# Kernel tuning notes

Measured on AMD Instinct MI355X. Metric: run time of the kernel, lower is better.

The kernel has to match this reference:

```python
import jax, jax.numpy as jnp
import numpy as np

B, N, FEAT, H, E, L = 4096, 64, 32, 128, 4, 3  # batch, node_num, node feat, hidden_dim, edge_dim, hidden_num


def setup_inputs() -> dict:
    key = jax.random.key(0)
    ks = jax.random.split(key, 12)
    s = 0.05
    x = jax.random.normal(ks[0], (B, N, FEAT), dtype=jnp.float32)
    adj = jax.random.uniform(ks[1], (B, E, N, N), dtype=jnp.float32)
    # per-node input/output embeddings (stacked over node index)
    in_w = jax.random.normal(ks[2], (N, FEAT, H), dtype=jnp.float32) * s
    in_b = jax.random.normal(ks[3], (N, H), dtype=jnp.float32) * s
    out_w = jax.random.normal(ks[4], (N, H, FEAT), dtype=jnp.float32) * s
    out_b = jax.random.normal(ks[5], (N, FEAT), dtype=jnp.float32) * s
    # relational GC weights per layer: (L, E, H, H) and bias (L, E, 1, H)
    gc_w = jax.random.normal(ks[6], (L, E, H, H), dtype=jnp.float32) * s
    gc_b = jax.random.normal(ks[7], (L, E, 1, H), dtype=jnp.float32) * s
    # GRU params, gate order [r, z, n] like torch
    w_ih = jax.random.normal(ks[8], (3 * H, H), dtype=jnp.float32) * s
    w_hh = jax.random.normal(ks[9], (3 * H, H), dtype=jnp.float32) * s
    b_ih = jax.random.normal(ks[10], (3 * H,), dtype=jnp.float32) * s
    b_hh = jax.random.normal(ks[11], (3 * H,), dtype=jnp.float32) * s
    return {"x": x, "adj": adj, "in_w": in_w, "in_b": in_b, "out_w": out_w,
            "out_b": out_b, "gc_w": gc_w, "gc_b": gc_b, "w_ih": w_ih,
            "w_hh": w_hh, "b_ih": b_ih, "b_hh": b_hh}


def _gru_step(xf, h, w_ih, w_hh, b_ih, b_hh):
    # xf, h: (B*N, H); single-timestep torch GRU cell
    gi = xf @ w_ih.T + b_ih
    gh = h @ w_hh.T + b_hh
    i_r, i_z, i_n = jnp.split(gi, 3, axis=-1)
    h_r, h_z, h_n = jnp.split(gh, 3, axis=-1)
    r = jax.nn.sigmoid(i_r + h_r)
    z = jax.nn.sigmoid(i_z + h_z)
    n = jnp.tanh(i_n + r * h_n)
    return (1.0 - z) * n + z * h


def reference(x, adj, in_w, in_b, out_w, out_b, gc_w, gc_b, w_ih, w_hh, b_ih, b_hh):
    # per-node input embedding: (B, N, FEAT) -> (B, N, H)
    h = jnp.einsum('bnd,ndh->bnh', x, in_w) + in_b
    hidden = h.reshape(-1, H)  # initial GRU hidden = embedded input
    cur = h
    for i in range(L):
        # relational GCN: per-edge-type projection + adjacency matmul + bias + relu + mean over edge types
        support = jnp.einsum('bid,edh->beih', cur, gc_w[i])
        out = jnp.einsum('beij,bejh->beih', adj, support) + gc_b[i]
        out = jax.nn.relu(out)
        agg = jnp.mean(out, axis=1)  # (B, N, H)
        hidden = _gru_step(agg.reshape(-1, H), hidden, w_ih, w_hh, b_ih, b_hh)
        cur = hidden.reshape(B, N, H)
    # per-node output embedding, zero-padded back to hidden width
    feats = jnp.einsum('bnh,nhd->bnd', cur, out_w) + out_b  # (B, N, FEAT)
    return jnp.pad(feats, ((0, 0), (0, 0), (0, H - FEAT)))
```

## Files before the change

kernel.cpp:

```cpp
#include <hip/hip_runtime.h>
#include <cstdint>

#define NBATCH 4096
#define NNODE  64
#define FEAT   32
#define H      128
#define NE     4
#define NL     3

typedef __attribute__((ext_vector_type(8))) short short8;
typedef __attribute__((ext_vector_type(4))) short short4v;
typedef __attribute__((ext_vector_type(4))) float f32x4;
typedef __attribute__((ext_vector_type(2))) float f32x2;
typedef unsigned long long u64;
typedef unsigned short ushort;

#define IMG_GC_ELEMS   (128 * 64)
#define IMG_GRU_ELEMS  (48 * 128)
#define IMG_GC_BYTES   (24 * IMG_GC_ELEMS * 2)
#define IMG_GRU_BYTES  (16 * IMG_GRU_ELEMS * 2)
#define WS_W_BYTES     (IMG_GC_BYTES + IMG_GRU_BYTES)
#define WIMG_SHORTS    (WS_W_BYTES / 2)
#define ADJ_IMG_ELEMS  4096
#define WS_FULL ((size_t)WS_W_BYTES + (size_t)NBATCH * NE * ADJ_IMG_ELEMS * 2)

__device__ __forceinline__ ushort f2b(float f) {
  union { float f; unsigned u; } v; v.f = f;
  unsigned u = v.u + 0x7FFFu + ((v.u >> 16) & 1u);
  return (ushort)(u >> 16);
}
__device__ __forceinline__ float b2f(ushort s) {
  union { unsigned u; float f; } v; v.u = ((unsigned)s) << 16;
  return v.f;
}
__device__ __forceinline__ unsigned cvtpk(float lo, float hi) {
  unsigned r;
  asm volatile("v_cvt_pk_bf16_f32 %0, %1, %2" : "=v"(r) : "v"(lo), "v"(hi));
  return r;
}
__device__ __forceinline__ u64 pk4(float a, float b, float c, float d) {
  return (u64)cvtpk(a, b) | ((u64)cvtpk(c, d) << 32);
}
__device__ __forceinline__ float sigm(float v) { return 1.0f / (1.0f + __expf(-v)); }
__device__ __forceinline__ float tanh_(float v) {
  v = fminf(fmaxf(v, -15.f), 15.f);
  float e = __expf(-2.f * v);
  return (1.f - e) / (1.f + e);
}
__device__ __forceinline__ int gidx128(int r, int g) { return r * 128 + ((g ^ (r & 7)) << 3); }
__device__ __forceinline__ int idx128(int r, int k) { return gidx128(r, k >> 3) + (k & 7); }
__device__ __forceinline__ int gidx64(int r, int g) { return r * 64 + (((g ^ (r & 7)) & 7) << 3); }

__device__ __forceinline__ short8 pack8f(const float* v) {
  union { unsigned u[4]; short8 s; } r;
  r.u[0] = cvtpk(v[0], v[1]); r.u[1] = cvtpk(v[2], v[3]);
  r.u[2] = cvtpk(v[4], v[5]); r.u[3] = cvtpk(v[6], v[7]);
  return r.s;
}

__device__ __forceinline__ void gll16(const void* g, void* l) {
  __builtin_amdgcn_global_load_lds(
      (const __attribute__((address_space(1))) unsigned int*)g,
      (__attribute__((address_space(3))) unsigned int*)l, 16, 0, 0);
}

#define STAGE(dst, src, NIT)                                             \
  do {                                                                   \
    _Pragma("unroll")                                                    \
    for (int it_ = 0; it_ < (NIT); ++it_) {                              \
      int off_ = (it_ * 4 + w) * 1024;                                   \
      gll16((const char*)(src) + off_ + lane * 16, (char*)(dst) + off_); \
    }                                                                    \
  } while (0)

#define MFMA16(A, B, C) __builtin_amdgcn_mfma_f32_16x16x32_bf16((A), (B), (C), 0, 0, 0)
#define GFRAG(base, off) (*(const short8*)&(base)[(off)])

__global__ __launch_bounds__(256, 2) void k_prep(
    const float* __restrict__ gc_w, const float* __restrict__ w_ih,
    const float* __restrict__ w_hh, ushort* __restrict__ ws)
{
  const int t = threadIdx.x;
  if (blockIdx.x < 24) {
    const int blk = blockIdx.x;
    const int kh = blk & 1, e = (blk >> 1) & 3, l = blk >> 3;
    const float* We = gc_w + (size_t)(l * NE + e) * H * H;
    ushort* dst = ws + (size_t)blk * IMG_GC_ELEMS;
    #pragma unroll
    for (int it = 0; it < 4; ++it) {
      int idx = t + it * 256;
      int r = idx >> 3, g = idx & 7;
      float v[8];
      #pragma unroll
      for (int j = 0; j < 8; ++j) v[j] = We[(kh * 64 + g * 8 + j) * H + r];
      *(short8*)&dst[gidx64(r, g)] = pack8f(v);
    }
  } else {
    const int blk = blockIdx.x - 24;
    const int c = blk & 7, m = blk >> 3;
    const float* Mat = m ? w_hh : w_ih;
    ushort* dst = ws + WIMG_SHORTS - IMG_GRU_BYTES / 2 + (size_t)blk * IMG_GRU_ELEMS;
    #pragma unroll
    for (int it = 0; it < 3; ++it) {
      int idx = t + it * 256;
      int rr = idx >> 4, g = idx & 15;
      int mrow = (rr >> 4) * H + 16 * c + (rr & 15);
      float v[8];
      #pragma unroll
      for (int j = 0; j < 8; ++j) v[j] = Mat[mrow * H + g * 8 + j];
      *(short8*)&dst[gidx128(rr, g)] = pack8f(v);
    }
  }
}

template <bool ADJIMG>
__global__ __launch_bounds__(256, 2) void k_inemb(
    const float* __restrict__ x, const float* __restrict__ in_w,
    const float* __restrict__ in_b, const float* __restrict__ adj,
    ushort* __restrict__ ws, float* __restrict__ out)
{
  __shared__ float s_wt[FEAT * H];
  __shared__ float s_x[64 * FEAT];
  const int t = threadIdx.x;
  const int n = blockIdx.x >> 6, bt = blockIdx.x & 63, b0 = bt * 64;
  const float* wsrc = in_w + (size_t)n * FEAT * H;
  #pragma unroll
  for (int it = 0; it < 4; ++it) {
    int i4 = t + it * 256;
    *(f32x4*)&s_wt[i4 * 4] = *(const f32x4*)&wsrc[i4 * 4];
  }
  {
    int r = t >> 2, q = t & 3;
    const float* xs = x + ((size_t)(b0 + r) * NNODE + n) * FEAT;
    *(f32x4*)&s_x[r * 32 + q * 8]     = *(const f32x4*)&xs[q * 8];
    *(f32x4*)&s_x[r * 32 + q * 8 + 4] = *(const f32x4*)&xs[q * 8 + 4];
  }
  __syncthreads();
  const int h2 = t & 63, rp = t >> 6;
  const float bi0 = in_b[n * H + 2 * h2], bi1 = in_b[n * H + 2 * h2 + 1];
  #pragma unroll 1
  for (int m = 0; m < 16; ++m) {
    int r = rp + 4 * m;
    float a0 = bi0, a1 = bi1;
    #pragma unroll
    for (int d = 0; d < 32; ++d) {
      float xv = s_x[r * 32 + d];
      f32x2 wv = *(const f32x2*)&s_wt[d * H + 2 * h2];
      a0 += xv * wv.x; a1 += xv * wv.y;
    }
    unsigned p = cvtpk(a0, a1);
    ushort* tail = (ushort*)(out + ((size_t)(b0 + r) * NNODE + n) * H + 64);
    *(unsigned*)(tail + 2 * h2) = p;
  }
  if (ADJIMG) {
    const float* ab = adj + (size_t)blockIdx.x * NE * NNODE * NNODE;
    ushort* dst = ws + WIMG_SHORTS + (size_t)blockIdx.x * NE * ADJ_IMG_ELEMS;
    #pragma unroll 1
    for (int q = 0; q < 8; ++q) {
      int gi = t + q * 256;
      int e = gi >> 9, idx = gi & 511, r = idx >> 3, g = idx & 7;
      const float* src = ab + e * 4096 + r * 64 + g * 8;
      float v[8];
      #pragma unroll
      for (int j = 0; j < 8; ++j) v[j] = src[j];
      *(short8*)&dst[e * ADJ_IMG_ELEMS + gidx64(r, g)] = pack8f(v);
    }
  }
}

template <bool ADJIMG>
__global__ __launch_bounds__(256, 2) void k_main(
    const float* __restrict__ adj,
    const float* __restrict__ gc_b,
    const float* __restrict__ b_ih, const float* __restrict__ b_hh,
    const ushort* __restrict__ wimg,
    float* __restrict__ out)
{
  __shared__ ushort s_u[8192];
  __shared__ ushort s_adj[4096];
  __shared__ float  s_bias[1280];

  const int t = threadIdx.x, b = blockIdx.x;
  const int w = t >> 6, lane = t & 63, lr = lane & 15, lq = lane >> 4;
  const int wm = w & 1, wn = w >> 1;
  float* outb = out + (size_t)b * NNODE * H;
  const ushort* img_gru = wimg + WIMG_SHORTS - IMG_GRU_BYTES / 2;
  const ushort* aimg = wimg + WIMG_SHORTS + (size_t)b * NE * ADJ_IMG_ELEMS;

  short8 cur[2][4];
  #pragma unroll
  for (int mt = 0; mt < 2; ++mt)
    #pragma unroll
    for (int ks = 0; ks < 4; ++ks)
      cur[mt][ks] = *(const short8*)((const ushort*)(outb + (size_t)(32 * wm + 16 * mt + lr) * H + 64) + 32 * ks + 8 * lq);
  #pragma unroll
  for (int it = 0; it < 3; ++it) {
    int idx = t + it * 256;
    s_bias[512 + idx] = (idx < 384) ? b_ih[idx] : b_hh[idx - 384];
  }
  __syncthreads();

  #pragma unroll 1
  for (int layer = 0; layer < NL; ++layer) {
    f32x4 agg[2][4];
    #pragma unroll
    for (int mt = 0; mt < 2; ++mt)
      #pragma unroll
      for (int nt = 0; nt < 4; ++nt) agg[mt][nt] = f32x4{0.f, 0.f, 0.f, 0.f};

    #pragma unroll 1
    for (int e = 0; e < NE; ++e) {
      const ushort* img_e = wimg + (size_t)((layer * NE + e) * 2) * IMG_GC_ELEMS;
      if (e == 0) {
        s_bias[t]       = gc_b[layer * 512 + t];
        s_bias[t + 256] = gc_b[layer * 512 + t + 256];
      }
      if (ADJIMG) {
        STAGE(s_adj, aimg + (size_t)e * ADJ_IMG_ELEMS, 2);
      } else {
        const float* adj_e = adj + (((size_t)b * NE + e) * NNODE * NNODE);
        #pragma unroll
        for (int it = 0; it < 2; ++it) {
          int idx = t + it * 256;
          int i = idx >> 3, g = idx & 7;
          const float* src = adj_e + i * 64 + g * 8;
          float v[8];
          #pragma unroll
          for (int j = 0; j < 8; ++j) v[j] = src[j];
          *(short8*)&s_adj[gidx64(i, g)] = pack8f(v);
        }
      }
      f32x4 Sacc[2][4];
      #pragma unroll
      for (int mt = 0; mt < 2; ++mt)
        #pragma unroll
        for (int nt = 0; nt < 4; ++nt) Sacc[mt][nt] = f32x4{0.f, 0.f, 0.f, 0.f};
      __builtin_amdgcn_s_setprio(1);
      #pragma unroll
      for (int kh = 0; kh < 2; ++kh) {
        const ushort* wb = img_e + (size_t)kh * IMG_GC_ELEMS;
        #pragma unroll
        for (int ks = 0; ks < 2; ++ks) {
          #pragma unroll
          for (int nt = 0; nt < 4; ++nt) {
            short8 bb = GFRAG(wb, gidx64(64 * wn + 16 * nt + lr, ks * 4 + lq));
            #pragma unroll
            for (int mt = 0; mt < 2; ++mt)
              Sacc[mt][nt] = MFMA16(cur[mt][2 * kh + ks], bb, Sacc[mt][nt]);
          }
        }
      }
      __builtin_amdgcn_s_setprio(0);
      #pragma unroll
      for (int mt = 0; mt < 2; ++mt) {
        int j0 = 32 * wm + 16 * mt + 4 * lq;
        #pragma unroll
        for (int nt = 0; nt < 4; ++nt) {
          int h = 64 * wn + 16 * nt + lr;
          *(u64*)&s_u[gidx64(h, j0 >> 3) + (j0 & 7)] =
              pk4(Sacc[mt][nt][0], Sacc[mt][nt][1], Sacc[mt][nt][2], Sacc[mt][nt][3]);
        }
      }
      __syncthreads();

      {
        f32x4 Oacc[2][4];
        #pragma unroll
        for (int mt = 0; mt < 2; ++mt)
          #pragma unroll
          for (int nt = 0; nt < 4; ++nt) Oacc[mt][nt] = f32x4{0.f, 0.f, 0.f, 0.f};
        __builtin_amdgcn_s_setprio(1);
        #pragma unroll
        for (int ks = 0; ks < 2; ++ks) {
          short8 a[2];
          #pragma unroll
          for (int mt = 0; mt < 2; ++mt)
            a[mt] = *(const short8*)&s_adj[gidx64(32 * wm + 16 * mt + lr, ks * 4 + lq)];
          #pragma unroll
          for (int nt = 0; nt < 4; ++nt) {
            short8 bb = *(const short8*)&s_u[gidx64(64 * wn + 16 * nt + lr, ks * 4 + lq)];
            #pragma unroll
            for (int mt = 0; mt < 2; ++mt)
              Oacc[mt][nt] = MFMA16(a[mt], bb, Oacc[mt][nt]);
          }
        }
        __builtin_amdgcn_s_setprio(0);
        #pragma unroll
        for (int mt = 0; mt < 2; ++mt)
          #pragma unroll
          for (int nt = 0; nt < 4; ++nt) {
            float bias = s_bias[e * 128 + 64 * wn + 16 * nt + lr];
            #pragma unroll
            for (int r = 0; r < 4; ++r)
              agg[mt][nt][r] += 0.25f * fmaxf(Oacc[mt][nt][r] + bias, 0.f);
          }
      }
      __syncthreads();
    }

    #pragma unroll
    for (int mt = 0; mt < 2; ++mt)
      #pragma unroll
      for (int nt = 0; nt < 4; ++nt) {
        int h = 64 * wn + 16 * nt + lr;
        #pragma unroll
        for (int r = 0; r < 4; ++r)
          s_u[idx128(32 * wm + 16 * mt + 4 * lq + r, h)] = f2b(agg[mt][nt][r]);
      }
    __syncthreads();

    #pragma unroll 1
    for (int p = 0; p < 4; ++p) {
      const int cc = 2 * p + wn;
      const ushort* ihg = img_gru + (size_t)cc * IMG_GRU_ELEMS;
      const ushort* hhg = img_gru + (size_t)(8 + cc) * IMG_GRU_ELEMS;
      short4v holdv[2];
      #pragma unroll
      for (int nst = 0; nst < 2; ++nst)
        holdv[nst] = *(const short4v*)((const ushort*)(outb + (size_t)(16 * (2 * wm + nst) + lr) * H + 64) + 16 * cc + 4 * lq);
      f32x4 gi[3][2], gh[3][2];
      #pragma unroll
      for (int tg = 0; tg < 3; ++tg)
        #pragma unroll
        for (int nst = 0; nst < 2; ++nst) {
          gi[tg][nst] = f32x4{0.f, 0.f, 0.f, 0.f};
          gh[tg][nst] = f32x4{0.f, 0.f, 0.f, 0.f};
        }
      __builtin_amdgcn_s_setprio(1);
      #pragma unroll
      for (int ks = 0; ks < 4; ++ks) {
        short8 bb[2];
        #pragma unroll
        for (int nst = 0; nst < 2; ++nst)
          bb[nst] = *(const short8*)&s_u[gidx128(16 * (2 * wm + nst) + lr, ks * 4 + lq)];
        #pragma unroll
        for (int tg = 0; tg < 3; ++tg) {
          short8 a = GFRAG(ihg, gidx128(16 * tg + lr, ks * 4 + lq));
          #pragma unroll
          for (int nst = 0; nst < 2; ++nst)
            gi[tg][nst] = MFMA16(a, bb[nst], gi[tg][nst]);
        }
      }
      #pragma unroll
      for (int ks = 0; ks < 4; ++ks) {
        #pragma unroll
        for (int tg = 0; tg < 3; ++tg) {
          short8 a = GFRAG(hhg, gidx128(16 * tg + lr, ks * 4 + lq));
          #pragma unroll
          for (int nst = 0; nst < 2; ++nst)
            gh[tg][nst] = MFMA16(a, cur[nst][ks], gh[tg][nst]);
        }
      }
      __builtin_amdgcn_s_setprio(0);
      #pragma unroll
      for (int nst = 0; nst < 2; ++nst) {
        int node = 16 * (2 * wm + nst) + lr;
        float hf[4];
        #pragma unroll
        for (int r = 0; r < 4; ++r) {
          int mH = 16 * cc + 4 * lq + r;
          float rg = sigm(gi[0][nst][r] + s_bias[512 + mH] + gh[0][nst][r] + s_bias[896 + mH]);
          float zg = sigm(gi[1][nst][r] + s_bias[640 + mH] + gh[1][nst][r] + s_bias[1024 + mH]);
          float ng = tanh_(gi[2][nst][r] + s_bias[768 + mH] + rg * (gh[2][nst][r] + s_bias[1152 + mH]));
          hf[r] = (1.f - zg) * ng + zg * b2f((ushort)holdv[nst][r]);
        }
        *(u64*)((ushort*)(outb + (size_t)node * H + 64) + 16 * cc + 4 * lq) =
            pk4(hf[0], hf[1], hf[2], hf[3]);
      }
    }
    __syncthreads();

    if (layer < 2) {
      #pragma unroll
      for (int mt = 0; mt < 2; ++mt)
        #pragma unroll
        for (int ks = 0; ks < 4; ++ks)
          cur[mt][ks] = *(const short8*)((const ushort*)(outb + (size_t)(32 * wm + 16 * mt + lr) * H + 64) + 32 * ks + 8 * lq);
    }
  }
}

__global__ __launch_bounds__(256, 2) void k_outemb(
    const float* __restrict__ out_w, const float* __restrict__ out_b,
    float* __restrict__ out)
{
  __shared__ float s_wt[H * FEAT];
  __shared__ float s_c[64 * 132];
  const int t = threadIdx.x;
  const int n = blockIdx.x >> 6, bt = blockIdx.x & 63, b0 = bt * 64;
  const float* wsrc = out_w + (size_t)n * H * FEAT;
  #pragma unroll
  for (int it = 0; it < 4; ++it) {
    int i4 = t + it * 256;
    *(f32x4*)&s_wt[i4 * 4] = *(const f32x4*)&wsrc[i4 * 4];
  }
  #pragma unroll
  for (int it = 0; it < 4; ++it) {
    int idx = t + it * 256;
    int r = idx >> 4, g = idx & 15;
    const ushort* tail = (const ushort*)(out + ((size_t)(b0 + r) * NNODE + n) * H + 64);
    short8 v = *(const short8*)(tail + g * 8);
    #pragma unroll
    for (int j = 0; j < 8; ++j) s_c[r * 132 + g * 8 + j] = b2f((ushort)v[j]);
  }
  __syncthreads();
  const int d = t & 31, rq = t >> 5;
  const float bias = out_b[n * FEAT + d];
  float accs[8];
  #pragma unroll
  for (int m = 0; m < 8; ++m) {
    int r = rq + 8 * m;
    float a = bias;
    #pragma unroll 8
    for (int k = 0; k < H; ++k) a += s_c[r * 132 + k] * s_wt[k * FEAT + d];
    accs[m] = a;
  }
  #pragma unroll
  for (int m = 0; m < 8; ++m) {
    int r = rq + 8 * m;
    out[((size_t)(b0 + r) * NNODE + n) * H + d] = accs[m];
  }
  #pragma unroll
  for (int q = 0; q < 6; ++q) {
    int idx = t + q * 256;
    int r = idx / 24, c4 = idx - r * 24;
    *(f32x4*)&out[((size_t)(b0 + r) * NNODE + n) * H + FEAT + c4 * 4] =
        f32x4{0.f, 0.f, 0.f, 0.f};
  }
}

extern "C" void kernel_launch(void* const* d_in, const int* in_sizes, int n_in,
                              void* d_out, int out_size, void* d_ws, size_t ws_size,
                              hipStream_t stream) {
  const float* x     = (const float*)d_in[0];
  const float* adj   = (const float*)d_in[1];
  const float* in_w  = (const float*)d_in[2];
  const float* in_b  = (const float*)d_in[3];
  const float* out_w = (const float*)d_in[4];
  const float* out_b = (const float*)d_in[5];
  const float* gc_w  = (const float*)d_in[6];
  const float* gc_b  = (const float*)d_in[7];
  const float* w_ih  = (const float*)d_in[8];
  const float* w_hh  = (const float*)d_in[9];
  const float* b_ih  = (const float*)d_in[10];
  const float* b_hh  = (const float*)d_in[11];
  (void)in_sizes; (void)n_in; (void)out_size;
  ushort* wimg = (ushort*)d_ws;
  const bool full = ws_size >= WS_FULL;
  hipLaunchKernelGGL(k_prep, dim3(40), dim3(256), 0, stream, gc_w, w_ih, w_hh, wimg);
  if (full) {
    hipLaunchKernelGGL(k_inemb<true>, dim3(NBATCH), dim3(256), 0, stream,
                       x, in_w, in_b, adj, wimg, (float*)d_out);
    hipLaunchKernelGGL(k_main<true>, dim3(NBATCH), dim3(256), 0, stream,
                       adj, gc_b, b_ih, b_hh, wimg, (float*)d_out);
  } else {
    hipLaunchKernelGGL(k_inemb<false>, dim3(NBATCH), dim3(256), 0, stream,
                       x, in_w, in_b, adj, wimg, (float*)d_out);
    hipLaunchKernelGGL(k_main<false>, dim3(NBATCH), dim3(256), 0, stream,
                       adj, gc_b, b_ih, b_hh, wimg, (float*)d_out);
  }
  hipLaunchKernelGGL(k_outemb, dim3(NBATCH), dim3(256), 0, stream, out_w, out_b, (float*)d_out);
}
```

Measured before the change: 854.0 us.

## Double-buffer GC weight images in LDS with async prefetch and vmcnt waits

```diff
diff --git a/kernel.cpp b/kernel.cpp
--- a/kernel.cpp
+++ b/kernel.cpp
@@ -72,6 +72,12 @@
       gll16((const char*)(src) + off_ + lane * 16, (char*)(dst) + off_); \
     }                                                                    \
   } while (0)
+
+#define BAR() do { asm volatile("s_waitcnt lgkmcnt(0)" ::: "memory"); \
+                   __builtin_amdgcn_s_barrier(); } while (0)
+#define VMW(N) do { asm volatile("s_waitcnt vmcnt(" #N ")" ::: "memory"); \
+                    __builtin_amdgcn_sched_barrier(0); } while (0)
+#define SB0() __builtin_amdgcn_sched_barrier(0)
 
 #define MFMA16(A, B, C) __builtin_amdgcn_mfma_f32_16x16x32_bf16((A), (B), (C), 0, 0, 0)
 #define GFRAG(base, off) (*(const short8*)&(base)[(off)])
@@ -176,8 +182,10 @@
     const ushort* __restrict__ wimg,
     float* __restrict__ out)
 {
+  __shared__ ushort s_w0[8192];
+  __shared__ ushort s_w1[8192];
+  __shared__ ushort s_adj[4096];
   __shared__ ushort s_u[8192];
-  __shared__ ushort s_adj[4096];
   __shared__ float  s_bias[1280];
 
   const int t = threadIdx.x, b = blockIdx.x;
@@ -187,6 +195,8 @@
   const ushort* img_gru = wimg + WIMG_SHORTS - IMG_GRU_BYTES / 2;
   const ushort* aimg = wimg + WIMG_SHORTS + (size_t)b * NE * ADJ_IMG_ELEMS;
 
+  STAGE(s_w0, wimg, 4);
+  STAGE(s_w1, wimg + IMG_GC_ELEMS, 4);
   short8 cur[2][4];
   #pragma unroll
   for (int mt = 0; mt < 2; ++mt)
@@ -211,12 +221,14 @@
     #pragma unroll 1
     for (int e = 0; e < NE; ++e) {
       const ushort* img_e = wimg + (size_t)((layer * NE + e) * 2) * IMG_GC_ELEMS;
+
       if (e == 0) {
         s_bias[t]       = gc_b[layer * 512 + t];
         s_bias[t + 256] = gc_b[layer * 512 + t + 256];
       }
       if (ADJIMG) {
         STAGE(s_adj, aimg + (size_t)e * ADJ_IMG_ELEMS, 2);
+        SB0();
       } else {
         const float* adj_e = adj + (((size_t)b * NE + e) * NNODE * NNODE);
         #pragma unroll
@@ -237,17 +249,28 @@
         for (int nt = 0; nt < 4; ++nt) Sacc[mt][nt] = f32x4{0.f, 0.f, 0.f, 0.f};
       __builtin_amdgcn_s_setprio(1);
       #pragma unroll
-      for (int kh = 0; kh < 2; ++kh) {
-        const ushort* wb = img_e + (size_t)kh * IMG_GC_ELEMS;
-        #pragma unroll
-        for (int ks = 0; ks < 2; ++ks) {
-          #pragma unroll
-          for (int nt = 0; nt < 4; ++nt) {
-            short8 bb = GFRAG(wb, gidx64(64 * wn + 16 * nt + lr, ks * 4 + lq));
-            #pragma unroll
-            for (int mt = 0; mt < 2; ++mt)
-              Sacc[mt][nt] = MFMA16(cur[mt][2 * kh + ks], bb, Sacc[mt][nt]);
-          }
+      for (int ks = 0; ks < 2; ++ks) {
+        #pragma unroll
+        for (int nt = 0; nt < 4; ++nt) {
+          short8 bb = *(const short8*)&s_w0[gidx64(64 * wn + 16 * nt + lr, ks * 4 + lq)];
+          #pragma unroll
+          for (int mt = 0; mt < 2; ++mt)
+            Sacc[mt][nt] = MFMA16(cur[mt][ks], bb, Sacc[mt][nt]);
+        }
+      }
+      __builtin_amdgcn_s_setprio(0);
+      if (ADJIMG) { VMW(2); BAR(); } else __syncthreads();
+
+      if (e < 3) { STAGE(s_w0, img_e + 2 * IMG_GC_ELEMS, 4); SB0(); }
+      __builtin_amdgcn_s_setprio(1);
+      #pragma unroll
+      for (int ks = 0; ks < 2; ++ks) {
+        #pragma unroll
+        for (int nt = 0; nt < 4; ++nt) {
+          short8 bb = *(const short8*)&s_w1[gidx64(64 * wn + 16 * nt + lr, ks * 4 + lq)];
+          #pragma unroll
+          for (int mt = 0; mt < 2; ++mt)
+            Sacc[mt][nt] = MFMA16(cur[mt][2 + ks], bb, Sacc[mt][nt]);
         }
       }
       __builtin_amdgcn_s_setprio(0);
@@ -261,8 +284,9 @@
               pk4(Sacc[mt][nt][0], Sacc[mt][nt][1], Sacc[mt][nt][2], Sacc[mt][nt][3]);
         }
       }
-      __syncthreads();
-
+      if (ADJIMG) { if (e < 3) { VMW(4); } else { VMW(0); } BAR(); } else __syncthreads();
+
+      if (e < 3) { STAGE(s_w1, img_e + 3 * IMG_GC_ELEMS, 4); SB0(); }
       {
         f32x4 Oacc[2][4];
         #pragma unroll
@@ -295,7 +319,7 @@
               agg[mt][nt][r] += 0.25f * fmaxf(Oacc[mt][nt][r] + bias, 0.f);
           }
       }
-      __syncthreads();
+      if (ADJIMG) { if (e < 3) { VMW(4); } BAR(); } else __syncthreads();
     }
 
     #pragma unroll
@@ -371,11 +395,15 @@
     __syncthreads();
 
     if (layer < 2) {
+      STAGE(s_w0, wimg + (size_t)((layer + 1) * NE * 2) * IMG_GC_ELEMS, 4);
+      STAGE(s_w1, wimg + (size_t)((layer + 1) * NE * 2 + 1) * IMG_GC_ELEMS, 4);
+      SB0();
       #pragma unroll
       for (int mt = 0; mt < 2; ++mt)
         #pragma unroll
         for (int ks = 0; ks < 4; ++ks)
           cur[mt][ks] = *(const short8*)((const ushort*)(outb + (size_t)(32 * wm + 16 * mt + lr) * H + 64) + 32 * ks + 8 * lq);
+      __syncthreads();
     }
   }
 }
```

Result: faster. 775.4 us (-9.2%).
